# Kernel tuning notes

Measured on AMD Instinct MI355X. Metric: run time of the kernel, lower is better.

Reference implementation:

```python
import math
import jax, jax.numpy as jnp
import numpy as np

B, T, C = 2, 2048, 2048
H, G = 16, 4          # n_head, n_group
HKV = H // G          # kv heads
HD = C // H           # head dim = 128

def setup_inputs() -> dict:
    key = jax.random.key(0)
    ks = jax.random.split(key, 4)
    s = 0.02  # realistic init scale
    return {
        "x": jax.random.normal(ks[0], (B, T, C), jnp.float32),
        "Wkv": jax.random.normal(ks[1], (C, 2 * C // G), jnp.float32) * s,
        "bkv": jnp.zeros((2 * C // G,), jnp.float32),
        "Wq": jax.random.normal(ks[2], (C, C), jnp.float32) * s,
        "bq": jnp.zeros((C,), jnp.float32),
        "Wp": jax.random.normal(ks[3], (C, C), jnp.float32) * s,
        "bp": jnp.zeros((C,), jnp.float32),
    }

def _expand_kv(t):
    # (B,T,HKV*HD) -> replicate each kv head G times -> (B,H,T,HD)
    t = t.reshape(B, T, HKV, HD)
    t = jnp.broadcast_to(t[:, :, None], (B, T, G, HKV, HD)).reshape(B, T, H, HD)
    return t.transpose(0, 2, 1, 3)

def reference(x, Wkv, bkv, Wq, bq, Wp, bp):
    kv = x @ Wkv + bkv                      # (B,T,2C/G)
    k, v = jnp.split(kv, 2, axis=-1)
    q = (x @ Wq + bq).reshape(B, T, H, HD).transpose(0, 2, 1, 3)  # (B,H,T,HD)
    k = _expand_kv(k)
    v = _expand_kv(v)
    att = jnp.einsum('bhqd,bhkd->bhqk', q, k) * (1.0 / math.sqrt(HD))
    mask = jnp.tril(jnp.ones((T, T), bool))
    att = jnp.where(mask, att, -jnp.inf)
    att = jax.nn.softmax(att, axis=-1)
    y = jnp.einsum('bhqk,bhkd->bhqd', att, v)
    y = y.transpose(0, 2, 1, 3).reshape(B, T, C)
    return y @ Wp + bp
```

## Files before the change

### kernel.cpp

```cpp
#include <hip/hip_runtime.h>

#define Bv 2
#define Tv 2048
#define Cv 2048
#define Hv 16
#define HKVv 4
#define HDv 128

typedef __attribute__((ext_vector_type(8))) __bf16 bf16x8;
typedef __attribute__((ext_vector_type(4))) float floatx4;

__device__ __forceinline__ unsigned short f2b(float f) {
  unsigned int x = __float_as_uint(f);
  x += 0x7fffu + ((x >> 16) & 1u);
  return (unsigned short)(x >> 16);
}

#define MFMA(a, b, c) __builtin_amdgcn_mfma_f32_16x16x32_bf16((a), (b), (c), 0, 0, 0)

__device__ __forceinline__ void gld_lds16(const void* g, void* l) {
  __builtin_amdgcn_global_load_lds((const __attribute__((address_space(1))) void*)g,
                                   (__attribute__((address_space(3))) void*)l, 16, 0, 0);
}

__global__ void cvt_kernel(const float* __restrict__ src, unsigned short* __restrict__ dst, int n4) {
  int i = blockIdx.x * blockDim.x + threadIdx.x;
  if (i < n4) {
    float4 f = ((const float4*)src)[i];
    ushort4 u;
    u.x = f2b(f.x); u.y = f2b(f.y); u.z = f2b(f.z); u.w = f2b(f.w);
    ((ushort4*)dst)[i] = u;
  }
}

__global__ void tcvt_kernel(const float* __restrict__ src, unsigned short* __restrict__ dst, int K, int N) {
  __shared__ float tile[32][33];
  int k0 = blockIdx.x * 32, n0 = blockIdx.y * 32;
  int tx = threadIdx.x, ty = threadIdx.y;
  for (int i = ty; i < 32; i += 8)
    tile[i][tx] = src[(size_t)(k0 + i) * N + n0 + tx];
  __syncthreads();
  for (int i = ty; i < 32; i += 8)
    dst[(size_t)(n0 + i) * K + k0 + tx] = f2b(tile[tx][i]);
}

__global__ __launch_bounds__(256) void gemm_qkv(
    const unsigned short* __restrict__ xb,
    const unsigned short* __restrict__ wq_t,
    const unsigned short* __restrict__ wkv_t,
    const float* __restrict__ bq, const float* __restrict__ bkv,
    unsigned short* __restrict__ qs,
    unsigned short* __restrict__ ks,
    unsigned short* __restrict__ vs) {
  __shared__ __align__(16) unsigned short Ash[128 * 32];
  __shared__ __align__(16) unsigned short Bsh[128 * 32];
  int tid = threadIdx.x;
  int wave = tid >> 6, lane = tid & 63;
  int c = lane & 15, quad = lane >> 4;
  int wr = (wave >> 1) * 64, wc = (wave & 1) * 64;
  int m0 = blockIdx.x * 128, n0 = blockIdx.y * 128;
  bool isq = (n0 < 2048);
  const unsigned short* wt = isq ? (wq_t + (size_t)n0 * 2048)
                                 : (wkv_t + (size_t)(n0 - 2048) * 2048);
  floatx4 zero4 = {0.f, 0.f, 0.f, 0.f};
  floatx4 acc[4][4];
#pragma unroll
  for (int i = 0; i < 4; i++)
#pragma unroll
    for (int j = 0; j < 4; j++) acc[i][j] = zero4;

  const unsigned short* Abase = xb + (size_t)m0 * 2048;
  int s0 = wave * 128 + lane, s1 = wave * 128 + 64 + lane;
  int r0 = s0 >> 2, kc0 = (s0 & 3) ^ (r0 & 3);
  int r1 = s1 >> 2, kc1 = (s1 & 3) ^ (r1 & 3);
  int swz3 = quad ^ (c & 3);

  for (int k0 = 0; k0 < 2048; k0 += 32) {
    gld_lds16(Abase + (size_t)r0 * 2048 + k0 + kc0 * 8, Ash + (size_t)(wave * 128) * 8);
    gld_lds16(Abase + (size_t)r1 * 2048 + k0 + kc1 * 8, Ash + (size_t)(wave * 128 + 64) * 8);
    gld_lds16(wt + (size_t)r0 * 2048 + k0 + kc0 * 8, Bsh + (size_t)(wave * 128) * 8);
    gld_lds16(wt + (size_t)r1 * 2048 + k0 + kc1 * 8, Bsh + (size_t)(wave * 128 + 64) * 8);
    __syncthreads();
    bf16x8 af[4], bfv[4];
#pragma unroll
    for (int i = 0; i < 4; i++)
      af[i] = *(const bf16x8*)(&Ash[(wr + i * 16 + c) * 32 + swz3 * 8]);
#pragma unroll
    for (int j = 0; j < 4; j++)
      bfv[j] = *(const bf16x8*)(&Bsh[(wc + j * 16 + c) * 32 + swz3 * 8]);
#pragma unroll
    for (int i = 0; i < 4; i++)
#pragma unroll
      for (int j = 0; j < 4; j++)
        acc[i][j] = MFMA(af[i], bfv[j], acc[i][j]);
    __syncthreads();
  }

#pragma unroll
  for (int i = 0; i < 4; i++) {
#pragma unroll
    for (int j = 0; j < 4; j++) {
#pragma unroll
      for (int r = 0; r < 4; r++) {
        int m = m0 + wr + i * 16 + quad * 4 + r;
        int n = n0 + wc + j * 16 + c;
        int bidx = m >> 11, t = m & 2047;
        float val = acc[i][j][r];
        if (isq) {
          val = (val + bq[n]) * 0.08838834764831845f;
          int hh = n >> 7, d = n & 127;
          qs[((size_t)((bidx * Hv + hh) * Tv) + t) * HDv + d] = f2b(val);
        } else {
          int n2 = n - 2048;
          val += bkv[n2];
          if (n2 < 512) {
            int hh = n2 >> 7, d = n2 & 127;
            ks[((size_t)((bidx * HKVv + hh) * Tv) + t) * HDv + d] = f2b(val);
          } else {
            int n3 = n2 - 512;
            int hh = n3 >> 7, d = n3 & 127;
            vs[((size_t)((bidx * HKVv + hh) * HDv) + d) * Tv + t] = f2b(val);
          }
        }
      }
    }
  }
}

__global__ __launch_bounds__(256, 4) void attn_kernel(
    const unsigned short* __restrict__ qs,
    const unsigned short* __restrict__ ks,
    const unsigned short* __restrict__ vs,
    unsigned short* __restrict__ ys) {
  __shared__ __align__(16) unsigned short Ksh[2][32 * 128];
  __shared__ __align__(16) unsigned short Vsh[2][128 * 32];
  __shared__ __align__(16) unsigned short Psh[4][16 * 32];

  int x = blockIdx.x, h = blockIdx.y, b = blockIdx.z;
  int qt = (h & 8) ? (31 - x) : x;
  int hkv = h & (HKVv - 1);
  int tid = threadIdx.x;
  int wave = tid >> 6, lane = tid & 63;
  int c = lane & 15, quad = lane >> 4;
  int q0w = qt * 64 + wave * 16;
  int qrow = q0w + c;
  int swzK = c & 7, swzV = c & 3;

  const unsigned short* qptr = qs + ((size_t)((b * Hv + h) * Tv) + q0w) * HDv;
  const unsigned short* kbase = ks + (size_t)((b * HKVv + hkv) * Tv) * HDv;
  const unsigned short* vbase = vs + (size_t)((b * HKVv + hkv) * HDv) * Tv;

  bf16x8 qf[4];
#pragma unroll
  for (int kc = 0; kc < 4; kc++)
    qf[kc] = *(const bf16x8*)(qptr + (size_t)c * HDv + kc * 32 + quad * 8);

  floatx4 zero4 = {0.f, 0.f, 0.f, 0.f};
  floatx4 o[8];
#pragma unroll
  for (int dt = 0; dt < 8; dt++) o[dt] = zero4;
  float M = -1e30f, L = 0.f;

  unsigned short* Pw = &Psh[wave][0];

  int kOff[2], vOff[2];
#pragma unroll
  for (int i = 0; i < 2; i++) {
    int s = wave * 128 + i * 64 + lane;
    int rk = s >> 4, gk = (s & 15) ^ (rk & 7);
    kOff[i] = rk * 128 + gk * 8;
    int rv = s >> 2, gv = (s & 3) ^ (rv & 3);
    vOff[i] = rv * Tv + gv * 8;
  }
  int ldsBase = (wave * 128) * 8;

  int ntiles = 2 * qt + 2;

#pragma unroll
  for (int i = 0; i < 2; i++) gld_lds16(kbase + kOff[i], &Ksh[0][0] + ldsBase + i * 512);
#pragma unroll
  for (int i = 0; i < 2; i++) gld_lds16(vbase + vOff[i], &Vsh[0][0] + ldsBase + i * 512);
  __syncthreads();

  for (int kt = 0; kt < ntiles; kt++) {
    int kv0 = kt * 32;
    int cur = kt & 1;
    if (kt + 1 < ntiles) {
      int kv1 = (kt + 1) * 32;
#pragma unroll
      for (int i = 0; i < 2; i++)
        gld_lds16(kbase + (size_t)kv1 * 128 + kOff[i], &Ksh[cur ^ 1][0] + ldsBase + i * 512);
#pragma unroll
      for (int i = 0; i < 2; i++)
        gld_lds16(vbase + kv1 + vOff[i], &Vsh[cur ^ 1][0] + ldsBase + i * 512);
    }

    if (kv0 <= q0w + 15) {
      const unsigned short* Kb = &Ksh[cur][0];
      const unsigned short* Vb = &Vsh[cur][0];
      floatx4 st[2] = {zero4, zero4};
#pragma unroll
      for (int kc = 0; kc < 4; kc++) {
#pragma unroll
        for (int sub = 0; sub < 2; sub++) {
          bf16x8 kf = *(const bf16x8*)(&Kb[(sub * 16 + c) * 128 + (((kc * 4 + quad) ^ swzK) * 8)]);
          st[sub] = MFMA(kf, qf[kc], st[sub]);
        }
      }
      if (kv0 + 31 > q0w) {
#pragma unroll
        for (int sub = 0; sub < 2; sub++) {
          int kvb = kv0 + sub * 16 + quad * 4;
#pragma unroll
          for (int r = 0; r < 4; r++)
            if (kvb + r > qrow) st[sub][r] = -1e30f;
        }
      }
      float mx = -1e30f;
#pragma unroll
      for (int sub = 0; sub < 2; sub++)
        mx = fmaxf(mx, fmaxf(fmaxf(st[sub][0], st[sub][1]), fmaxf(st[sub][2], st[sub][3])));
      mx = fmaxf(mx, __shfl_xor(mx, 16));
      mx = fmaxf(mx, __shfl_xor(mx, 32));
      float Mn = fmaxf(M, mx);
      float al = __expf(M - Mn);
      M = Mn;
      float l = 0.f;
#pragma unroll
      for (int sub = 0; sub < 2; sub++) {
        float p0 = __expf(st[sub][0] - Mn);
        float p1 = __expf(st[sub][1] - Mn);
        float p2 = __expf(st[sub][2] - Mn);
        float p3 = __expf(st[sub][3] - Mn);
        l += (p0 + p1) + (p2 + p3);
        unsigned int lo = (unsigned int)f2b(p0) | ((unsigned int)f2b(p1) << 16);
        unsigned int hi = (unsigned int)f2b(p2) | ((unsigned int)f2b(p3) << 16);
        int g = (sub * 2 + (quad >> 1)) ^ swzV;
        *(uint2*)(&Pw[c * 32 + g * 8 + (quad & 1) * 4]) = make_uint2(lo, hi);
      }
      l += __shfl_xor(l, 16);
      l += __shfl_xor(l, 32);
      L = L * al + l;
#pragma unroll
      for (int dt = 0; dt < 8; dt++) o[dt] *= al;
      bf16x8 pf = *(const bf16x8*)(&Pw[c * 32 + ((quad ^ swzV) * 8)]);
#pragma unroll
      for (int dt = 0; dt < 8; dt++) {
        bf16x8 vf = *(const bf16x8*)(&Vb[(dt * 16 + c) * 32 + ((quad ^ swzV) * 8)]);
        o[dt] = MFMA(vf, pf, o[dt]);
      }
    }
    __syncthreads();
  }

  float Li = 1.0f / L;
  size_t rowbase = ((size_t)(b * Tv + qrow)) * Cv + h * HDv;
#pragma unroll
  for (int dt = 0; dt < 8; dt++) {
    unsigned int lo = (unsigned int)f2b(o[dt][0] * Li) | ((unsigned int)f2b(o[dt][1] * Li) << 16);
    unsigned int hi2 = (unsigned int)f2b(o[dt][2] * Li) | ((unsigned int)f2b(o[dt][3] * Li) << 16);
    *(uint2*)(&ys[rowbase + dt * 16 + quad * 4]) = make_uint2(lo, hi2);
  }
}

__global__ __launch_bounds__(256) void gemm_proj(
    const unsigned short* __restrict__ ys,
    const unsigned short* __restrict__ wp_t,
    const float* __restrict__ bp,
    float* __restrict__ out) {
  __shared__ __align__(16) unsigned short Ash[128 * 32];
  __shared__ __align__(16) unsigned short Bsh[128 * 32];
  int tid = threadIdx.x;
  int wave = tid >> 6, lane = tid & 63;
  int c = lane & 15, quad = lane >> 4;
  int wr = (wave >> 1) * 64, wc = (wave & 1) * 64;
  int m0 = blockIdx.x * 128, n0 = blockIdx.y * 128;
  floatx4 zero4 = {0.f, 0.f, 0.f, 0.f};
  floatx4 acc[4][4];
#pragma unroll
  for (int i = 0; i < 4; i++)
#pragma unroll
    for (int j = 0; j < 4; j++) acc[i][j] = zero4;

  const unsigned short* Abase = ys + (size_t)m0 * 2048;
  const unsigned short* Bbase = wp_t + (size_t)n0 * 2048;
  int s0 = wave * 128 + lane, s1 = wave * 128 + 64 + lane;
  int r0 = s0 >> 2, kc0 = (s0 & 3) ^ (r0 & 3);
  int r1 = s1 >> 2, kc1 = (s1 & 3) ^ (r1 & 3);
  int swz3 = quad ^ (c & 3);

  for (int k0 = 0; k0 < 2048; k0 += 32) {
    gld_lds16(Abase + (size_t)r0 * 2048 + k0 + kc0 * 8, Ash + (size_t)(wave * 128) * 8);
    gld_lds16(Abase + (size_t)r1 * 2048 + k0 + kc1 * 8, Ash + (size_t)(wave * 128 + 64) * 8);
    gld_lds16(Bbase + (size_t)r0 * 2048 + k0 + kc0 * 8, Bsh + (size_t)(wave * 128) * 8);
    gld_lds16(Bbase + (size_t)r1 * 2048 + k0 + kc1 * 8, Bsh + (size_t)(wave * 128 + 64) * 8);
    __syncthreads();
    bf16x8 af[4], bfv[4];
#pragma unroll
    for (int i = 0; i < 4; i++)
      af[i] = *(const bf16x8*)(&Ash[(wr + i * 16 + c) * 32 + swz3 * 8]);
#pragma unroll
    for (int j = 0; j < 4; j++)
      bfv[j] = *(const bf16x8*)(&Bsh[(wc + j * 16 + c) * 32 + swz3 * 8]);
#pragma unroll
    for (int i = 0; i < 4; i++)
#pragma unroll
      for (int j = 0; j < 4; j++)
        acc[i][j] = MFMA(af[i], bfv[j], acc[i][j]);
    __syncthreads();
  }

#pragma unroll
  for (int i = 0; i < 4; i++) {
#pragma unroll
    for (int j = 0; j < 4; j++) {
#pragma unroll
      for (int r = 0; r < 4; r++) {
        int m = m0 + wr + i * 16 + quad * 4 + r;
        int n = n0 + wc + j * 16 + c;
        out[(size_t)m * 2048 + n] = acc[i][j][r] + bp[n];
      }
    }
  }
}

extern "C" void kernel_launch(void* const* d_in, const int* in_sizes, int n_in,
                              void* d_out, int out_size, void* d_ws, size_t ws_size,
                              hipStream_t stream) {
  (void)in_sizes; (void)n_in; (void)out_size; (void)ws_size;
  const float* x   = (const float*)d_in[0];
  const float* Wkv = (const float*)d_in[1];
  const float* bkv = (const float*)d_in[2];
  const float* Wq  = (const float*)d_in[3];
  const float* bq  = (const float*)d_in[4];
  const float* Wp  = (const float*)d_in[5];
  const float* bp  = (const float*)d_in[6];
  float* out = (float*)d_out;

  char* ws = (char*)d_ws;
  unsigned short* xb    = (unsigned short*)(ws + 0);
  unsigned short* wq_t  = (unsigned short*)(ws + 16777216);
  unsigned short* wkv_t = (unsigned short*)(ws + 25165824);
  unsigned short* wp_t  = (unsigned short*)(ws + 29360128);
  unsigned short* qs    = (unsigned short*)(ws + 37748736);
  unsigned short* ks    = (unsigned short*)(ws + 54525952);
  unsigned short* vs    = (unsigned short*)(ws + 58720256);
  unsigned short* ysbuf = (unsigned short*)(ws + 62914560);

  cvt_kernel<<<8192, 256, 0, stream>>>(x, xb, 2097152);
  tcvt_kernel<<<dim3(64, 64), dim3(32, 8), 0, stream>>>(Wq, wq_t, 2048, 2048);
  tcvt_kernel<<<dim3(64, 32), dim3(32, 8), 0, stream>>>(Wkv, wkv_t, 2048, 1024);
  tcvt_kernel<<<dim3(64, 64), dim3(32, 8), 0, stream>>>(Wp, wp_t, 2048, 2048);
  gemm_qkv<<<dim3(32, 24), 256, 0, stream>>>(xb, wq_t, wkv_t, bq, bkv, qs, ks, vs);
  attn_kernel<<<dim3(32, 16, 2), 256, 0, stream>>>(qs, ks, vs, ysbuf);
  gemm_proj<<<dim3(32, 16), 256, 0, stream>>>(ysbuf, wp_t, bp, out);
}
```

Baseline: 369.7 us.

## Double-buffer LDS tiles in QKV and projection GEMMs to overlap loads

```diff
diff --git a/kernel.cpp b/kernel.cpp
--- a/kernel.cpp
+++ b/kernel.cpp
@@ -52,8 +52,8 @@
     unsigned short* __restrict__ qs,
     unsigned short* __restrict__ ks,
     unsigned short* __restrict__ vs) {
-  __shared__ __align__(16) unsigned short Ash[128 * 32];
-  __shared__ __align__(16) unsigned short Bsh[128 * 32];
+  __shared__ __align__(16) unsigned short Ash[2][128 * 32];
+  __shared__ __align__(16) unsigned short Bsh[2][128 * 32];
   int tid = threadIdx.x;
   int wave = tid >> 6, lane = tid & 63;
   int c = lane & 15, quad = lane >> 4;
@@ -74,20 +74,30 @@
   int r0 = s0 >> 2, kc0 = (s0 & 3) ^ (r0 & 3);
   int r1 = s1 >> 2, kc1 = (s1 & 3) ^ (r1 & 3);
   int swz3 = quad ^ (c & 3);
-
-  for (int k0 = 0; k0 < 2048; k0 += 32) {
-    gld_lds16(Abase + (size_t)r0 * 2048 + k0 + kc0 * 8, Ash + (size_t)(wave * 128) * 8);
-    gld_lds16(Abase + (size_t)r1 * 2048 + k0 + kc1 * 8, Ash + (size_t)(wave * 128 + 64) * 8);
-    gld_lds16(wt + (size_t)r0 * 2048 + k0 + kc0 * 8, Bsh + (size_t)(wave * 128) * 8);
-    gld_lds16(wt + (size_t)r1 * 2048 + k0 + kc1 * 8, Bsh + (size_t)(wave * 128 + 64) * 8);
-    __syncthreads();
+  int dA0 = (wave * 128) * 8, dA1 = (wave * 128 + 64) * 8;
+
+  gld_lds16(Abase + (size_t)r0 * 2048 + kc0 * 8, &Ash[0][0] + dA0);
+  gld_lds16(Abase + (size_t)r1 * 2048 + kc1 * 8, &Ash[0][0] + dA1);
+  gld_lds16(wt + (size_t)r0 * 2048 + kc0 * 8, &Bsh[0][0] + dA0);
+  gld_lds16(wt + (size_t)r1 * 2048 + kc1 * 8, &Bsh[0][0] + dA1);
+  __syncthreads();
+
+  for (int it = 0; it < 64; it++) {
+    int cur = it & 1;
+    if (it + 1 < 64) {
+      int k1 = (it + 1) * 32;
+      gld_lds16(Abase + (size_t)r0 * 2048 + k1 + kc0 * 8, &Ash[cur ^ 1][0] + dA0);
+      gld_lds16(Abase + (size_t)r1 * 2048 + k1 + kc1 * 8, &Ash[cur ^ 1][0] + dA1);
+      gld_lds16(wt + (size_t)r0 * 2048 + k1 + kc0 * 8, &Bsh[cur ^ 1][0] + dA0);
+      gld_lds16(wt + (size_t)r1 * 2048 + k1 + kc1 * 8, &Bsh[cur ^ 1][0] + dA1);
+    }
     bf16x8 af[4], bfv[4];
 #pragma unroll
     for (int i = 0; i < 4; i++)
-      af[i] = *(const bf16x8*)(&Ash[(wr + i * 16 + c) * 32 + swz3 * 8]);
+      af[i] = *(const bf16x8*)(&Ash[cur][(wr + i * 16 + c) * 32 + swz3 * 8]);
 #pragma unroll
     for (int j = 0; j < 4; j++)
-      bfv[j] = *(const bf16x8*)(&Bsh[(wc + j * 16 + c) * 32 + swz3 * 8]);
+      bfv[j] = *(const bf16x8*)(&Bsh[cur][(wc + j * 16 + c) * 32 + swz3 * 8]);
 #pragma unroll
     for (int i = 0; i < 4; i++)
 #pragma unroll
@@ -268,8 +278,8 @@
     const unsigned short* __restrict__ wp_t,
     const float* __restrict__ bp,
     float* __restrict__ out) {
-  __shared__ __align__(16) unsigned short Ash[128 * 32];
-  __shared__ __align__(16) unsigned short Bsh[128 * 32];
+  __shared__ __align__(16) unsigned short Ash[2][128 * 32];
+  __shared__ __align__(16) unsigned short Bsh[2][128 * 32];
   int tid = threadIdx.x;
   int wave = tid >> 6, lane = tid & 63;
   int c = lane & 15, quad = lane >> 4;
@@ -288,20 +298,30 @@
   int r0 = s0 >> 2, kc0 = (s0 & 3) ^ (r0 & 3);
   int r1 = s1 >> 2, kc1 = (s1 & 3) ^ (r1 & 3);
   int swz3 = quad ^ (c & 3);
-
-  for (int k0 = 0; k0 < 2048; k0 += 32) {
-    gld_lds16(Abase + (size_t)r0 * 2048 + k0 + kc0 * 8, Ash + (size_t)(wave * 128) * 8);
-    gld_lds16(Abase + (size_t)r1 * 2048 + k0 + kc1 * 8, Ash + (size_t)(wave * 128 + 64) * 8);
-    gld_lds16(Bbase + (size_t)r0 * 2048 + k0 + kc0 * 8, Bsh + (size_t)(wave * 128) * 8);
-    gld_lds16(Bbase + (size_t)r1 * 2048 + k0 + kc1 * 8, Bsh + (size_t)(wave * 128 + 64) * 8);
-    __syncthreads();
+  int dA0 = (wave * 128) * 8, dA1 = (wave * 128 + 64) * 8;
+
+  gld_lds16(Abase + (size_t)r0 * 2048 + kc0 * 8, &Ash[0][0] + dA0);
+  gld_lds16(Abase + (size_t)r1 * 2048 + kc1 * 8, &Ash[0][0] + dA1);
+  gld_lds16(Bbase + (size_t)r0 * 2048 + kc0 * 8, &Bsh[0][0] + dA0);
+  gld_lds16(Bbase + (size_t)r1 * 2048 + kc1 * 8, &Bsh[0][0] + dA1);
+  __syncthreads();
+
+  for (int it = 0; it < 64; it++) {
+    int cur = it & 1;
+    if (it + 1 < 64) {
+      int k1 = (it + 1) * 32;
+      gld_lds16(Abase + (size_t)r0 * 2048 + k1 + kc0 * 8, &Ash[cur ^ 1][0] + dA0);
+      gld_lds16(Abase + (size_t)r1 * 2048 + k1 + kc1 * 8, &Ash[cur ^ 1][0] + dA1);
+      gld_lds16(Bbase + (size_t)r0 * 2048 + k1 + kc0 * 8, &Bsh[cur ^ 1][0] + dA0);
+      gld_lds16(Bbase + (size_t)r1 * 2048 + k1 + kc1 * 8, &Bsh[cur ^ 1][0] + dA1);
+    }
     bf16x8 af[4], bfv[4];
 #pragma unroll
     for (int i = 0; i < 4; i++)
-      af[i] = *(const bf16x8*)(&Ash[(wr + i * 16 + c) * 32 + swz3 * 8]);
+      af[i] = *(const bf16x8*)(&Ash[cur][(wr + i * 16 + c) * 32 + swz3 * 8]);
 #pragma unroll
     for (int j = 0; j < 4; j++)
-      bfv[j] = *(const bf16x8*)(&Bsh[(wc + j * 16 + c) * 32 + swz3 * 8]);
+      bfv[j] = *(const bf16x8*)(&Bsh[cur][(wc + j * 16 + c) * 32 + swz3 * 8]);
 #pragma unroll
     for (int i = 0; i < 4; i++)
 #pragma unroll
```

New measurement: 349.6 us. 5.4% less time.
